# Kernel tuning notes

Hardware: AMD Instinct MI355X
Metric: run time of the kernel (lower is better)

## Reference

```python
import jax, jax.numpy as jnp
import numpy as np

B, C, H, W = 32, 512, 32, 32
HEADS = 8
HD = C // HEADS  # 64
BN_EPS = 1e-5


def setup_inputs() -> dict:
    key = jax.random.key(0)
    ks = jax.random.split(key, 8)
    s = 0.02  # trunc_normal std for Linear weights
    x = jax.random.normal(ks[0], (B, C, H, W), jnp.float32)
    Wq = jax.random.normal(ks[1], (C, C), jnp.float32) * s
    Wk = jax.random.normal(ks[2], (C, C), jnp.float32) * s
    Wv = jax.random.normal(ks[3], (C, C), jnp.float32) * s
    # depthwise 3x3 kernel, kaiming fan_out (fan_out = 3*3*1 per group)
    dw_w = jax.random.normal(ks[4], (C, 1, 3, 3), jnp.float32) * np.sqrt(2.0 / 9.0)
    bn_gamma = jnp.ones((C,), jnp.float32)
    bn_beta = jnp.zeros((C,), jnp.float32)
    temperature = jnp.ones((HEADS, 1, 1), jnp.float32)
    Wp = jax.random.normal(ks[5], (C, C), jnp.float32) * s
    bp = jnp.zeros((C,), jnp.float32)
    return {"x": x, "Wq": Wq, "Wk": Wk, "Wv": Wv, "dw_w": dw_w,
            "bn_gamma": bn_gamma, "bn_beta": bn_beta,
            "temperature": temperature, "Wp": Wp, "bp": bp}


def _l2norm(t):
    # torch F.normalize: x / max(||x||, eps)
    n = jnp.sqrt(jnp.sum(t * t, axis=-1, keepdims=True))
    return t / jnp.maximum(n, 1e-12)


def _forward(x, Wq, Wk, Wv, dw_w, bn_gamma, bn_beta, temperature, Wp, bp):
    b, c, h, w = x.shape
    n = h * w
    x_flat = x.transpose(0, 2, 3, 1).reshape(b, n, c)  # [B,N,C]

    q = (x_flat @ Wq.T).reshape(b, n, HEADS, HD).transpose(0, 2, 3, 1)  # [B,h,d,N]
    k = (x_flat @ Wk.T).reshape(b, n, HEADS, HD).transpose(0, 2, 3, 1)
    q = _l2norm(q)
    k = _l2norm(k)

    attn = jnp.einsum('bhdn,bhen->bhde', q, k) * temperature  # [B,h,d,d]
    attn = jax.nn.softmax(attn, axis=-1)

    v_content = x_flat @ Wv.T  # [B,N,C]

    # gated value path: DWConv -> BatchNorm (batch stats, train mode) -> SiLU
    g = jax.lax.conv_general_dilated(
        x, dw_w, window_strides=(1, 1), padding=((1, 1), (1, 1)),
        feature_group_count=c, dimension_numbers=('NCHW', 'OIHW', 'NCHW'))
    mu = jnp.mean(g, axis=(0, 2, 3), keepdims=True)
    var = jnp.var(g, axis=(0, 2, 3), keepdims=True)
    g = (g - mu) * jax.lax.rsqrt(var + BN_EPS)
    g = g * bn_gamma[None, :, None, None] + bn_beta[None, :, None, None]
    g = g * jax.nn.sigmoid(g)  # SiLU
    v_gate = g.transpose(0, 2, 3, 1).reshape(b, n, c)

    v = (v_content * v_gate).reshape(b, n, HEADS, HD).transpose(0, 2, 3, 1)  # [B,h,d,N]
    out = jnp.einsum('bhde,bhen->bhdn', attn, v)  # [B,h,d,N]
    out = out.transpose(0, 3, 1, 2).reshape(b, n, c)  # [B,N,C]
    out = out @ Wp.T + bp
    return out.reshape(b, h, w, c).transpose(0, 3, 1, 2)  # [B,C,H,W]


def reference(x, Wq, Wk, Wv, dw_w, bn_gamma, bn_beta, temperature, Wp, bp):
    return _forward(x, Wq, Wk, Wv, dw_w, bn_gamma, bn_beta, temperature, Wp, bp)
```

## Files before the change

kernel.cpp:

```cpp
#include <hip/hip_runtime.h>
#include <stdint.h>

#define BATCH 32
#define CCH   512
#define NPIX  1024
#define HEADS 8
#define QKV_M 1536

typedef short bf16x8 __attribute__((ext_vector_type(8)));
typedef float f32x4 __attribute__((ext_vector_type(4)));

__device__ inline float bf2f(unsigned short u) {
  union { float f; uint32_t i; } t; t.i = ((uint32_t)u) << 16; return t.f;
}
__device__ inline unsigned short f2bf(float f) {
  union { float f; uint32_t u; } t; t.f = f;
  uint32_t u = t.u;
  return (unsigned short)((u + 0x7FFFu + ((u >> 16) & 1u)) >> 16);
}

__device__ inline void gl_lds16(const unsigned short* g, unsigned short* l) {
  __builtin_amdgcn_global_load_lds(
      (const __attribute__((address_space(1))) uint32_t*)g,
      (__attribute__((address_space(3))) uint32_t*)l, 16, 0, 0);
}

__global__ void convert_w(const float* __restrict__ Wq, const float* __restrict__ Wk,
                          const float* __restrict__ Wv, const float* __restrict__ Wp,
                          unsigned short* __restrict__ wcat,
                          unsigned short* __restrict__ wpb) {
  int i = (blockIdx.x * 256 + threadIdx.x) * 4;
  union { ushort4 u4; unsigned short s[4]; } o;
  f32x4 a;
  a = *(const f32x4*)&Wq[i];
  for (int j = 0; j < 4; j++) o.s[j] = f2bf(a[j]);
  *(ushort4*)&wcat[i] = o.u4;
  a = *(const f32x4*)&Wk[i];
  for (int j = 0; j < 4; j++) o.s[j] = f2bf(a[j]);
  *(ushort4*)&wcat[CCH * CCH + i] = o.u4;
  a = *(const f32x4*)&Wv[i];
  for (int j = 0; j < 4; j++) o.s[j] = f2bf(a[j]);
  *(ushort4*)&wcat[2 * CCH * CCH + i] = o.u4;
  a = *(const f32x4*)&Wp[i];
  for (int j = 0; j < 4; j++) o.s[j] = f2bf(a[j]);
  *(ushort4*)&wpb[i] = o.u4;
}

__global__ void transpose_f2b(const float* __restrict__ in,
                              unsigned short* __restrict__ out, int R, int Cc) {
  __shared__ float tile[32][33];
  int b = blockIdx.z;
  int c0 = blockIdx.x * 32;
  int r0 = blockIdx.y * 32;
  const float* inb = in + (size_t)b * R * Cc;
  unsigned short* outb = out + (size_t)b * R * Cc;
  int tx = threadIdx.x, ty = threadIdx.y;
  for (int i = 0; i < 4; i++) {
    int r = ty + i * 8;
    tile[r][tx] = inb[(size_t)(r0 + r) * Cc + c0 + tx];
  }
  __syncthreads();
  for (int i = 0; i < 4; i++) {
    int r = ty + i * 8;
    outb[(size_t)(c0 + r) * R + r0 + tx] = f2bf(tile[tx][r]);
  }
}

template <bool OUT_F32>
__launch_bounds__(256)
__global__ void gemm_bt(const unsigned short* __restrict__ A,
                        const unsigned short* __restrict__ X,
                        void* __restrict__ Cout,
                        const float* __restrict__ bias,
                        int M, int N, int K) {
  __shared__ __align__(16) unsigned short As[128 * 64];
  __shared__ __align__(16) unsigned short Bs[128 * 64];
  int b  = blockIdx.z;
  int m0 = blockIdx.y * 128;
  int n0 = blockIdx.x * 128;
  const unsigned short* Xb = X + (size_t)b * N * K;
  int tid = threadIdx.x;
  int lane = tid & 63;
  int wave = tid >> 6;
  int wm = wave >> 1, wn = wave & 1;
  int quad = lane >> 4, l16 = lane & 15;

  f32x4 acc[4][4];
  f32x4 zero = {0.f, 0.f, 0.f, 0.f};
  for (int i = 0; i < 4; i++)
    for (int j = 0; j < 4; j++) acc[i][j] = zero;

  int r8 = lane >> 3;
  int sw = ((lane & 7) ^ r8) * 8;
  const unsigned short* Ag = A  + (size_t)(m0 + wave * 32 + r8) * K + sw;
  const unsigned short* Xg = Xb + (size_t)(n0 + wave * 32 + r8) * K + sw;
  unsigned short* Al = &As[wave * 32 * 64];
  unsigned short* Bl = &Bs[wave * 32 * 64];

  for (int k0 = 0; k0 < K; k0 += 64) {
    for (int i = 0; i < 4; i++) {
      gl_lds16(Ag + k0 + i * 8 * K, Al + i * 8 * 64);
      gl_lds16(Xg + k0 + i * 8 * K, Bl + i * 8 * 64);
    }
    __syncthreads();
    bf16x8 af[2][4], bfr[2][4];
    for (int ks = 0; ks < 2; ks++)
      for (int i = 0; i < 4; i++) {
        int ch = ((ks * 4 + quad) ^ (l16 & 7)) * 8;
        af[ks][i]  = *(const bf16x8*)&As[(wm * 64 + i * 16 + l16) * 64 + ch];
        bfr[ks][i] = *(const bf16x8*)&Bs[(wn * 64 + i * 16 + l16) * 64 + ch];
      }
    for (int ks = 0; ks < 2; ks++)
      for (int i = 0; i < 4; i++)
        for (int j = 0; j < 4; j++)
          acc[i][j] = __builtin_amdgcn_mfma_f32_16x16x32_bf16(
              af[ks][i], bfr[ks][j], acc[i][j], 0, 0, 0);
    __syncthreads();
  }

  for (int i = 0; i < 4; i++) {
    int gmb = m0 + wm * 64 + i * 16 + quad * 4;
    for (int j = 0; j < 4; j++) {
      int gn = n0 + wn * 64 + j * 16 + l16;
      for (int r = 0; r < 4; r++) {
        int gm = gmb + r;
        float v = acc[i][j][r];
        if (OUT_F32) {
          v += bias[gm];
          ((float*)Cout)[(size_t)b * M * N + (size_t)gm * N + gn] = v;
        } else {
          ((unsigned short*)Cout)[(size_t)b * M * N + (size_t)gm * N + gn] = f2bf(v);
        }
      }
    }
  }
}

__global__ void dw_stats(const float* __restrict__ x,
                         const float* __restrict__ wgt,
                         float* __restrict__ s1, float* __restrict__ s2) {
  int c = blockIdx.x, b = blockIdx.y;
  __shared__ __align__(16) float plane[NPIX];
  const float* xp = x + ((size_t)b * CCH + c) * NPIX;
  *(f32x4*)&plane[threadIdx.x * 4] = *(const f32x4*)&xp[threadIdx.x * 4];
  __syncthreads();
  float w[9];
  for (int i = 0; i < 9; i++) w[i] = wgt[c * 9 + i];
  float a1 = 0.f, a2 = 0.f;
  for (int pi = 0; pi < 4; pi++) {
    int p = threadIdx.x + pi * 256;
    int h = p >> 5, wc = p & 31;
    float v = 0.f;
    for (int dh = -1; dh <= 1; dh++)
      for (int dw = -1; dw <= 1; dw++) {
        int hh = h + dh, ww = wc + dw;
        if (hh >= 0 && hh < 32 && ww >= 0 && ww < 32)
          v += w[(dh + 1) * 3 + dw + 1] * plane[hh * 32 + ww];
      }
    a1 += v; a2 += v * v;
  }
  for (int off = 32; off > 0; off >>= 1) {
    a1 += __shfl_down(a1, off);
    a2 += __shfl_down(a2, off);
  }
  __shared__ float r1[4], r2[4];
  int wv = threadIdx.x >> 6;
  if ((threadIdx.x & 63) == 0) { r1[wv] = a1; r2[wv] = a2; }
  __syncthreads();
  if (threadIdx.x == 0) {
    atomicAdd(&s1[c], r1[0] + r1[1] + r1[2] + r1[3]);
    atomicAdd(&s2[c], r2[0] + r2[1] + r2[2] + r2[3]);
  }
}

__global__ void gate_apply(const float* __restrict__ x,
                           const float* __restrict__ wgt,
                           const float* __restrict__ s1, const float* __restrict__ s2,
                           const float* __restrict__ gamma,
                           const float* __restrict__ beta,
                           unsigned short* __restrict__ qkv) {
  int c = blockIdx.x, b = blockIdx.y;
  __shared__ __align__(16) float plane[NPIX];
  const float* xp = x + ((size_t)b * CCH + c) * NPIX;
  unsigned short* vp = qkv + ((size_t)b * QKV_M + 2 * CCH + c) * NPIX;
  *(f32x4*)&plane[threadIdx.x * 4] = *(const f32x4*)&xp[threadIdx.x * 4];
  __syncthreads();
  float w[9];
  for (int i = 0; i < 9; i++) w[i] = wgt[c * 9 + i];
  const float invn = 1.f / 32768.f;
  float mean = s1[c] * invn;
  float var = fmaxf(s2[c] * invn - mean * mean, 0.f);
  float rstd = rsqrtf(var + 1e-5f);
  float ga = gamma[c], be = beta[c];
  for (int pi = 0; pi < 4; pi++) {
    int p = threadIdx.x + pi * 256;
    int h = p >> 5, wc = p & 31;
    float val = 0.f;
    for (int dh = -1; dh <= 1; dh++)
      for (int dw = -1; dw <= 1; dw++) {
        int hh = h + dh, ww = wc + dw;
        if (hh >= 0 && hh < 32 && ww >= 0 && ww < 32)
          val += w[(dh + 1) * 3 + dw + 1] * plane[hh * 32 + ww];
      }
    float g = (val - mean) * rstd * ga + be;
    float sg = g / (1.f + __expf(-g));
    vp[p] = f2bf(bf2f(vp[p]) * sg);
  }
}

__launch_bounds__(256)
__global__ void attn_s(const unsigned short* __restrict__ qkv,
                       const float* __restrict__ temp,
                       unsigned short* __restrict__ P) {
  int bh = blockIdx.x;
  int b = bh >> 3, h = bh & 7;
  const unsigned short* Q = qkv + ((size_t)b * QKV_M + h * 64) * NPIX;
  const unsigned short* K = Q + (size_t)CCH * NPIX;
  int tid = threadIdx.x, lane = tid & 63, wave = tid >> 6;
  int quad = lane >> 4, l16 = lane & 15;

  __shared__ __align__(16) float Sf[64][65];
  __shared__ float qq[64], kk[64], invq[64], invk[64];
  __shared__ float redm[4][64], reds[4][64];

  f32x4 zero = {0.f, 0.f, 0.f, 0.f};
  f32x4 acc[4], accQ = zero, accK = zero;
  for (int j = 0; j < 4; j++) acc[j] = zero;
  for (int n0 = 0; n0 < NPIX; n0 += 32) {
    bf16x8 a  = *(const bf16x8*)&Q[(size_t)(wave * 16 + l16) * NPIX + n0 + quad * 8];
    bf16x8 ak = *(const bf16x8*)&K[(size_t)(wave * 16 + l16) * NPIX + n0 + quad * 8];
    accQ = __builtin_amdgcn_mfma_f32_16x16x32_bf16(a, a, accQ, 0, 0, 0);
    accK = __builtin_amdgcn_mfma_f32_16x16x32_bf16(ak, ak, accK, 0, 0, 0);
    for (int j = 0; j < 4; j++) {
      bf16x8 bb = *(const bf16x8*)&K[(size_t)(j * 16 + l16) * NPIX + n0 + quad * 8];
      acc[j] = __builtin_amdgcn_mfma_f32_16x16x32_bf16(a, bb, acc[j], 0, 0, 0);
    }
  }
  for (int j = 0; j < 4; j++)
    for (int r = 0; r < 4; r++)
      Sf[wave * 16 + quad * 4 + r][j * 16 + l16] = acc[j][r];
  for (int r = 0; r < 4; r++)
    if (l16 == quad * 4 + r) {
      qq[wave * 16 + l16] = accQ[r];
      kk[wave * 16 + l16] = accK[r];
    }
  __syncthreads();
  if (tid < 64) invq[tid] = 1.f / fmaxf(sqrtf(qq[tid]), 1e-12f);
  else if (tid < 128) invk[tid - 64] = 1.f / fmaxf(sqrtf(kk[tid - 64]), 1e-12f);
  __syncthreads();

  int row = tid & 63, seg = tid >> 6;
  float fq = temp[h] * invq[row];
  float v[16], pm = -1e30f;
  for (int i = 0; i < 16; i++) {
    v[i] = Sf[row][seg * 16 + i] * fq * invk[seg * 16 + i];
    pm = fmaxf(pm, v[i]);
  }
  redm[seg][row] = pm;
  __syncthreads();
  float m = fmaxf(fmaxf(redm[0][row], redm[1][row]),
                  fmaxf(redm[2][row], redm[3][row]));
  float ps = 0.f;
  for (int i = 0; i < 16; i++) { v[i] = __expf(v[i] - m); ps += v[i]; }
  reds[seg][row] = ps;
  __syncthreads();
  float inv = 1.f / (reds[0][row] + reds[1][row] + reds[2][row] + reds[3][row]);
  union { uint4 q4[2]; unsigned short s[16]; } u;
  for (int i = 0; i < 16; i++) u.s[i] = f2bf(v[i] * inv);
  unsigned short* Pp = P + ((size_t)bh * 64 + row) * 64 + seg * 16;
  *(uint4*)&Pp[0] = u.q4[0];
  *(uint4*)&Pp[8] = u.q4[1];
}

__launch_bounds__(256)
__global__ void attn_o(const unsigned short* __restrict__ qkv,
                       const unsigned short* __restrict__ P,
                       unsigned short* __restrict__ aoT) {
  int blk = blockIdx.x;
  int nc = blk & 3, bh = blk >> 2;
  int b = bh >> 3, h = bh & 7;
  const unsigned short* V = qkv + ((size_t)b * QKV_M + 2 * CCH + h * 64) * NPIX;
  unsigned short* Ob = aoT + (size_t)b * NPIX * CCH + h * 64;
  int tid = threadIdx.x, lane = tid & 63, wave = tid >> 6;
  int quad = lane >> 4, l16 = lane & 15;

  __shared__ __align__(16) unsigned short Vt[4][16][72];
  __shared__ __align__(16) unsigned short Ot[4][16][72];

  const unsigned short* Pb = P + (size_t)bh * 64 * 64;
  bf16x8 Pf[4][2];
  for (int j = 0; j < 4; j++)
    for (int ks = 0; ks < 2; ks++)
      Pf[j][ks] = *(const bf16x8*)&Pb[(j * 16 + l16) * 64 + ks * 32 + quad * 8];

  f32x4 zero = {0.f, 0.f, 0.f, 0.f};
  int e1 = lane >> 1, noff = (lane & 1) * 8;
  int nbase = nc * 256 + wave * 64;
  int orow = lane >> 3, ocol = (lane & 7) * 8;

  union { uint4 q; unsigned short s[8]; } g0, g1, c0, c1;
  g0.q = *(const uint4*)&V[(size_t)e1 * NPIX + nbase + noff];
  g1.q = *(const uint4*)&V[(size_t)(e1 + 32) * NPIX + nbase + noff];
#pragma unroll
  for (int nt = 0; nt < 4; nt++) {
    int n0 = nbase + nt * 16;
    c0 = g0; c1 = g1;
    if (nt < 3) {
      g0.q = *(const uint4*)&V[(size_t)e1 * NPIX + n0 + 16 + noff];
      g1.q = *(const uint4*)&V[(size_t)(e1 + 32) * NPIX + n0 + 16 + noff];
    }
    for (int jj = 0; jj < 8; jj++) {
      Vt[wave][noff + jj][e1]      = c0.s[jj];
      Vt[wave][noff + jj][e1 + 32] = c1.s[jj];
    }
    bf16x8 Af0 = *(const bf16x8*)&Vt[wave][l16][quad * 8];
    bf16x8 Af1 = *(const bf16x8*)&Vt[wave][l16][32 + quad * 8];
    f32x4 oacc[4];
    for (int j = 0; j < 4; j++) {
      oacc[j] = __builtin_amdgcn_mfma_f32_16x16x32_bf16(Af0, Pf[j][0], zero, 0, 0, 0);
      oacc[j] = __builtin_amdgcn_mfma_f32_16x16x32_bf16(Af1, Pf[j][1], oacc[j], 0, 0, 0);
    }
    for (int j = 0; j < 4; j++)
      for (int r = 0; r < 4; r++)
        Ot[wave][quad * 4 + r][j * 16 + l16] = f2bf(oacc[j][r]);
    uint4 o0 = *(const uint4*)&Ot[wave][orow][ocol];
    uint4 o1 = *(const uint4*)&Ot[wave][orow + 8][ocol];
    *(uint4*)&Ob[(size_t)(n0 + orow) * CCH + ocol] = o0;
    *(uint4*)&Ob[(size_t)(n0 + orow + 8) * CCH + ocol] = o1;
  }
}

extern "C" void kernel_launch(void* const* d_in, const int* in_sizes, int n_in,
                              void* d_out, int out_size, void* d_ws, size_t ws_size,
                              hipStream_t stream) {
  const float* x     = (const float*)d_in[0];
  const float* Wq    = (const float*)d_in[1];
  const float* Wk    = (const float*)d_in[2];
  const float* Wv    = (const float*)d_in[3];
  const float* dww   = (const float*)d_in[4];
  const float* gamma = (const float*)d_in[5];
  const float* beta  = (const float*)d_in[6];
  const float* temp  = (const float*)d_in[7];
  const float* Wp    = (const float*)d_in[8];
  const float* bp    = (const float*)d_in[9];
  float* out = (float*)d_out;

  char* ws = (char*)d_ws;
  unsigned short* wcat = (unsigned short*)ws;
  unsigned short* wpb  = wcat + (size_t)QKV_M * CCH;
  float* s1 = (float*)(wpb + (size_t)CCH * CCH);
  float* s2 = s1 + CCH;
  unsigned short* Pbuf = (unsigned short*)(s2 + CCH);
  char* dyn = (char*)(Pbuf + (size_t)BATCH * HEADS * 64 * 64);
  size_t fixed = (size_t)(dyn - ws);
  size_t per_b = ((size_t)NPIX * CCH + (size_t)QKV_M * NPIX) * 2;
  int BC = BATCH;
  while (BC > 1 && fixed + (size_t)BC * per_b > ws_size) BC >>= 1;
  unsigned short* xT  = (unsigned short*)dyn;
  unsigned short* qkv = xT + (size_t)BC * NPIX * CCH;

  convert_w<<<CCH * CCH / 1024, 256, 0, stream>>>(Wq, Wk, Wv, Wp, wcat, wpb);
  hipMemsetAsync(s1, 0, 2 * CCH * sizeof(float), stream);
  dw_stats<<<dim3(CCH, BATCH), 256, 0, stream>>>(x, dww, s1, s2);

  for (int b0 = 0; b0 < BATCH; b0 += BC) {
    const float* xc = x + (size_t)b0 * CCH * NPIX;
    float* outc = out + (size_t)b0 * CCH * NPIX;
    transpose_f2b<<<dim3(NPIX / 32, CCH / 32, BC), dim3(32, 8), 0, stream>>>(
        xc, xT, CCH, NPIX);
    gemm_bt<false><<<dim3(NPIX / 128, QKV_M / 128, BC), 256, 0, stream>>>(
        wcat, xT, qkv, nullptr, QKV_M, NPIX, CCH);
    attn_s<<<BC * HEADS, 256, 0, stream>>>(qkv, temp, Pbuf);
    gate_apply<<<dim3(CCH, BC), 256, 0, stream>>>(xc, dww, s1, s2, gamma, beta, qkv);
    attn_o<<<BC * HEADS * 4, 256, 0, stream>>>(qkv, Pbuf, xT);
    gemm_bt<true><<<dim3(NPIX / 128, CCH / 128, BC), 256, 0, stream>>>(
        wpb, xT, outc, bp, CCH, NPIX, CCH);
  }
}
```

Before: 336.2 us.

## Fuse BN-SiLU gating into QKV GEMM epilogue and split attn_s along N

The depthwise conv output is now stored once as bf16 while the BN statistics are gathered, and a small kernel precomputes the per-channel BN scale and shift. The QKV GEMM uses 256-row tiles and applies the SiLU gate to the V rows in its epilogue, which removes the separate gate_apply pass that recomputed the conv and reread and rewrote V. attn_s now splits the pixel dimension across its four waves and sums the partial scores in shared memory, so each wave has more MFMA work. The cost is an extra bf16 gate buffer of B*C*N elements, more workspace (which can shrink the batch chunk), and higher register pressure in the larger GEMM tile.

```diff
diff --git a/kernel.cpp b/kernel.cpp
--- a/kernel.cpp
+++ b/kernel.cpp
@@ -66,82 +66,14 @@
   }
 }
 
-template <bool OUT_F32>
-__launch_bounds__(256)
-__global__ void gemm_bt(const unsigned short* __restrict__ A,
-                        const unsigned short* __restrict__ X,
-                        void* __restrict__ Cout,
-                        const float* __restrict__ bias,
-                        int M, int N, int K) {
-  __shared__ __align__(16) unsigned short As[128 * 64];
-  __shared__ __align__(16) unsigned short Bs[128 * 64];
-  int b  = blockIdx.z;
-  int m0 = blockIdx.y * 128;
-  int n0 = blockIdx.x * 128;
-  const unsigned short* Xb = X + (size_t)b * N * K;
-  int tid = threadIdx.x;
-  int lane = tid & 63;
-  int wave = tid >> 6;
-  int wm = wave >> 1, wn = wave & 1;
-  int quad = lane >> 4, l16 = lane & 15;
-
-  f32x4 acc[4][4];
-  f32x4 zero = {0.f, 0.f, 0.f, 0.f};
-  for (int i = 0; i < 4; i++)
-    for (int j = 0; j < 4; j++) acc[i][j] = zero;
-
-  int r8 = lane >> 3;
-  int sw = ((lane & 7) ^ r8) * 8;
-  const unsigned short* Ag = A  + (size_t)(m0 + wave * 32 + r8) * K + sw;
-  const unsigned short* Xg = Xb + (size_t)(n0 + wave * 32 + r8) * K + sw;
-  unsigned short* Al = &As[wave * 32 * 64];
-  unsigned short* Bl = &Bs[wave * 32 * 64];
-
-  for (int k0 = 0; k0 < K; k0 += 64) {
-    for (int i = 0; i < 4; i++) {
-      gl_lds16(Ag + k0 + i * 8 * K, Al + i * 8 * 64);
-      gl_lds16(Xg + k0 + i * 8 * K, Bl + i * 8 * 64);
-    }
-    __syncthreads();
-    bf16x8 af[2][4], bfr[2][4];
-    for (int ks = 0; ks < 2; ks++)
-      for (int i = 0; i < 4; i++) {
-        int ch = ((ks * 4 + quad) ^ (l16 & 7)) * 8;
-        af[ks][i]  = *(const bf16x8*)&As[(wm * 64 + i * 16 + l16) * 64 + ch];
-        bfr[ks][i] = *(const bf16x8*)&Bs[(wn * 64 + i * 16 + l16) * 64 + ch];
-      }
-    for (int ks = 0; ks < 2; ks++)
-      for (int i = 0; i < 4; i++)
-        for (int j = 0; j < 4; j++)
-          acc[i][j] = __builtin_amdgcn_mfma_f32_16x16x32_bf16(
-              af[ks][i], bfr[ks][j], acc[i][j], 0, 0, 0);
-    __syncthreads();
-  }
-
-  for (int i = 0; i < 4; i++) {
-    int gmb = m0 + wm * 64 + i * 16 + quad * 4;
-    for (int j = 0; j < 4; j++) {
-      int gn = n0 + wn * 64 + j * 16 + l16;
-      for (int r = 0; r < 4; r++) {
-        int gm = gmb + r;
-        float v = acc[i][j][r];
-        if (OUT_F32) {
-          v += bias[gm];
-          ((float*)Cout)[(size_t)b * M * N + (size_t)gm * N + gn] = v;
-        } else {
-          ((unsigned short*)Cout)[(size_t)b * M * N + (size_t)gm * N + gn] = f2bf(v);
-        }
-      }
-    }
-  }
-}
-
-__global__ void dw_stats(const float* __restrict__ x,
-                         const float* __restrict__ wgt,
-                         float* __restrict__ s1, float* __restrict__ s2) {
+__global__ void conv_store(const float* __restrict__ x,
+                           const float* __restrict__ wgt,
+                           unsigned short* __restrict__ gbuf,
+                           float* __restrict__ s1, float* __restrict__ s2) {
   int c = blockIdx.x, b = blockIdx.y;
   __shared__ __align__(16) float plane[NPIX];
   const float* xp = x + ((size_t)b * CCH + c) * NPIX;
+  unsigned short* gp = gbuf + ((size_t)b * CCH + c) * NPIX;
   *(f32x4*)&plane[threadIdx.x * 4] = *(const f32x4*)&xp[threadIdx.x * 4];
   __syncthreads();
   float w[9];
@@ -158,6 +90,7 @@
           v += w[(dh + 1) * 3 + dw + 1] * plane[hh * 32 + ww];
       }
     a1 += v; a2 += v * v;
+    gp[p] = f2bf(v);
   }
   for (int off = 32; off > 0; off >>= 1) {
     a1 += __shfl_down(a1, off);
@@ -173,38 +106,146 @@
   }
 }
 
-__global__ void gate_apply(const float* __restrict__ x,
-                           const float* __restrict__ wgt,
-                           const float* __restrict__ s1, const float* __restrict__ s2,
-                           const float* __restrict__ gamma,
-                           const float* __restrict__ beta,
-                           unsigned short* __restrict__ qkv) {
-  int c = blockIdx.x, b = blockIdx.y;
-  __shared__ __align__(16) float plane[NPIX];
-  const float* xp = x + ((size_t)b * CCH + c) * NPIX;
-  unsigned short* vp = qkv + ((size_t)b * QKV_M + 2 * CCH + c) * NPIX;
-  *(f32x4*)&plane[threadIdx.x * 4] = *(const f32x4*)&xp[threadIdx.x * 4];
-  __syncthreads();
-  float w[9];
-  for (int i = 0; i < 9; i++) w[i] = wgt[c * 9 + i];
+__global__ void bn_coef(const float* __restrict__ s1, const float* __restrict__ s2,
+                        const float* __restrict__ gamma, const float* __restrict__ beta,
+                        float2* __restrict__ coef) {
+  int c = blockIdx.x * 256 + threadIdx.x;
   const float invn = 1.f / 32768.f;
   float mean = s1[c] * invn;
   float var = fmaxf(s2[c] * invn - mean * mean, 0.f);
-  float rstd = rsqrtf(var + 1e-5f);
-  float ga = gamma[c], be = beta[c];
-  for (int pi = 0; pi < 4; pi++) {
-    int p = threadIdx.x + pi * 256;
-    int h = p >> 5, wc = p & 31;
-    float val = 0.f;
-    for (int dh = -1; dh <= 1; dh++)
-      for (int dw = -1; dw <= 1; dw++) {
-        int hh = h + dh, ww = wc + dw;
-        if (hh >= 0 && hh < 32 && ww >= 0 && ww < 32)
-          val += w[(dh + 1) * 3 + dw + 1] * plane[hh * 32 + ww];
+  float sc = gamma[c] * rsqrtf(var + 1e-5f);
+  coef[c] = make_float2(sc, beta[c] - mean * sc);
+}
+
+__launch_bounds__(256, 2)
+__global__ void gemm_qkv(const unsigned short* __restrict__ A,
+                         const unsigned short* __restrict__ X,
+                         unsigned short* __restrict__ Cout,
+                         const unsigned short* __restrict__ gbuf,
+                         const float2* __restrict__ coef,
+                         int N, int K) {
+  __shared__ __align__(16) unsigned short As[256 * 64];
+  __shared__ __align__(16) unsigned short Bs[128 * 64];
+  int b  = blockIdx.z;
+  int m0 = blockIdx.y * 256;
+  int n0 = blockIdx.x * 128;
+  const unsigned short* Xb = X + (size_t)b * N * K;
+  int tid = threadIdx.x;
+  int lane = tid & 63;
+  int wave = tid >> 6;
+  int wm = wave >> 1, wn = wave & 1;
+  int quad = lane >> 4, l16 = lane & 15;
+
+  f32x4 acc[8][4];
+  f32x4 zero = {0.f, 0.f, 0.f, 0.f};
+  for (int i = 0; i < 8; i++)
+    for (int j = 0; j < 4; j++) acc[i][j] = zero;
+
+  int r8 = lane >> 3;
+  int sw = ((lane & 7) ^ r8) * 8;
+  const unsigned short* Ag = A  + (size_t)(m0 + wave * 64 + r8) * K + sw;
+  const unsigned short* Xg = Xb + (size_t)(n0 + wave * 32 + r8) * K + sw;
+  unsigned short* Al = &As[wave * 64 * 64];
+  unsigned short* Bl = &Bs[wave * 32 * 64];
+
+  for (int k0 = 0; k0 < K; k0 += 64) {
+    for (int i = 0; i < 8; i++) gl_lds16(Ag + k0 + i * 8 * K, Al + i * 8 * 64);
+    for (int i = 0; i < 4; i++) gl_lds16(Xg + k0 + i * 8 * K, Bl + i * 8 * 64);
+    __syncthreads();
+    for (int ks = 0; ks < 2; ks++) {
+      int ch = ((ks * 4 + quad) ^ (l16 & 7)) * 8;
+      bf16x8 af[8], bfr[4];
+      for (int i = 0; i < 8; i++)
+        af[i] = *(const bf16x8*)&As[(wm * 128 + i * 16 + l16) * 64 + ch];
+      for (int j = 0; j < 4; j++)
+        bfr[j] = *(const bf16x8*)&Bs[(wn * 64 + j * 16 + l16) * 64 + ch];
+      for (int i = 0; i < 8; i++)
+        for (int j = 0; j < 4; j++)
+          acc[i][j] = __builtin_amdgcn_mfma_f32_16x16x32_bf16(af[i], bfr[j], acc[i][j], 0, 0, 0);
+    }
+    __syncthreads();
+  }
+
+  bool gate = (m0 >= 2 * CCH);
+  for (int i = 0; i < 8; i++) {
+    int gm0 = m0 + wm * 128 + i * 16 + quad * 4;
+    for (int r = 0; r < 4; r++) {
+      int gm = gm0 + r;
+      float sc = 0.f, sh = 0.f;
+      if (gate) { float2 cf = coef[gm - 2 * CCH]; sc = cf.x; sh = cf.y; }
+      for (int j = 0; j < 4; j++) {
+        int gn = n0 + wn * 64 + j * 16 + l16;
+        float v = acc[i][j][r];
+        if (gate) {
+          float gg = bf2f(gbuf[((size_t)b * CCH + (gm - 2 * CCH)) * NPIX + gn]);
+          float gi = gg * sc + sh;
+          v *= gi / (1.f + __expf(-gi));
+        }
+        Cout[(size_t)b * QKV_M * N + (size_t)gm * N + gn] = f2bf(v);
       }
-    float g = (val - mean) * rstd * ga + be;
-    float sg = g / (1.f + __expf(-g));
-    vp[p] = f2bf(bf2f(vp[p]) * sg);
+    }
+  }
+}
+
+__launch_bounds__(256)
+__global__ void gemm_proj(const unsigned short* __restrict__ A,
+                          const unsigned short* __restrict__ X,
+                          float* __restrict__ Cout,
+                          const float* __restrict__ bias,
+                          int M, int N, int K) {
+  __shared__ __align__(16) unsigned short As[128 * 64];
+  __shared__ __align__(16) unsigned short Bs[128 * 64];
+  int b  = blockIdx.z;
+  int m0 = blockIdx.y * 128;
+  int n0 = blockIdx.x * 128;
+  const unsigned short* Xb = X + (size_t)b * N * K;
+  int tid = threadIdx.x;
+  int lane = tid & 63;
+  int wave = tid >> 6;
+  int wm = wave >> 1, wn = wave & 1;
+  int quad = lane >> 4, l16 = lane & 15;
+
+  f32x4 acc[4][4];
+  f32x4 zero = {0.f, 0.f, 0.f, 0.f};
+  for (int i = 0; i < 4; i++)
+    for (int j = 0; j < 4; j++) acc[i][j] = zero;
+
+  int r8 = lane >> 3;
+  int sw = ((lane & 7) ^ r8) * 8;
+  const unsigned short* Ag = A  + (size_t)(m0 + wave * 32 + r8) * K + sw;
+  const unsigned short* Xg = Xb + (size_t)(n0 + wave * 32 + r8) * K + sw;
+  unsigned short* Al = &As[wave * 32 * 64];
+  unsigned short* Bl = &Bs[wave * 32 * 64];
+
+  for (int k0 = 0; k0 < K; k0 += 64) {
+    for (int i = 0; i < 4; i++) {
+      gl_lds16(Ag + k0 + i * 8 * K, Al + i * 8 * 64);
+      gl_lds16(Xg + k0 + i * 8 * K, Bl + i * 8 * 64);
+    }
+    __syncthreads();
+    for (int ks = 0; ks < 2; ks++) {
+      int ch = ((ks * 4 + quad) ^ (l16 & 7)) * 8;
+      bf16x8 af[4], bfr[4];
+      for (int i = 0; i < 4; i++) {
+        af[i]  = *(const bf16x8*)&As[(wm * 64 + i * 16 + l16) * 64 + ch];
+        bfr[i] = *(const bf16x8*)&Bs[(wn * 64 + i * 16 + l16) * 64 + ch];
+      }
+      for (int i = 0; i < 4; i++)
+        for (int j = 0; j < 4; j++)
+          acc[i][j] = __builtin_amdgcn_mfma_f32_16x16x32_bf16(af[i], bfr[j], acc[i][j], 0, 0, 0);
+    }
+    __syncthreads();
+  }
+
+  for (int i = 0; i < 4; i++) {
+    int gmb = m0 + wm * 64 + i * 16 + quad * 4;
+    for (int j = 0; j < 4; j++) {
+      int gn = n0 + wn * 64 + j * 16 + l16;
+      for (int r = 0; r < 4; r++) {
+        int gm = gmb + r;
+        Cout[(size_t)b * M * N + (size_t)gm * N + gn] = acc[i][j][r] + bias[gm];
+      }
+    }
   }
 }
 
@@ -219,41 +260,58 @@
   int tid = threadIdx.x, lane = tid & 63, wave = tid >> 6;
   int quad = lane >> 4, l16 = lane & 15;
 
-  __shared__ __align__(16) float Sf[64][65];
-  __shared__ float qq[64], kk[64], invq[64], invk[64];
+  __shared__ float Sp[4][64][68];
+  __shared__ float qqp[4][64], kkp[4][64];
   __shared__ float redm[4][64], reds[4][64];
+  __shared__ float invq[64], invk[64];
 
   f32x4 zero = {0.f, 0.f, 0.f, 0.f};
-  f32x4 acc[4], accQ = zero, accK = zero;
-  for (int j = 0; j < 4; j++) acc[j] = zero;
-  for (int n0 = 0; n0 < NPIX; n0 += 32) {
-    bf16x8 a  = *(const bf16x8*)&Q[(size_t)(wave * 16 + l16) * NPIX + n0 + quad * 8];
-    bf16x8 ak = *(const bf16x8*)&K[(size_t)(wave * 16 + l16) * NPIX + n0 + quad * 8];
-    accQ = __builtin_amdgcn_mfma_f32_16x16x32_bf16(a, a, accQ, 0, 0, 0);
-    accK = __builtin_amdgcn_mfma_f32_16x16x32_bf16(ak, ak, accK, 0, 0, 0);
-    for (int j = 0; j < 4; j++) {
-      bf16x8 bb = *(const bf16x8*)&K[(size_t)(j * 16 + l16) * NPIX + n0 + quad * 8];
-      acc[j] = __builtin_amdgcn_mfma_f32_16x16x32_bf16(a, bb, acc[j], 0, 0, 0);
-    }
-  }
-  for (int j = 0; j < 4; j++)
+  f32x4 acc[4][4], accQ[4], accK[4];
+  for (int i = 0; i < 4; i++) {
+    accQ[i] = zero; accK[i] = zero;
+    for (int j = 0; j < 4; j++) acc[i][j] = zero;
+  }
+  for (int nc = 0; nc < 8; nc++) {
+    int n0 = wave * 256 + nc * 32;
+    bf16x8 qa[4], ka[4];
+    for (int i = 0; i < 4; i++) {
+      qa[i] = *(const bf16x8*)&Q[(size_t)(i * 16 + l16) * NPIX + n0 + quad * 8];
+      ka[i] = *(const bf16x8*)&K[(size_t)(i * 16 + l16) * NPIX + n0 + quad * 8];
+    }
+    for (int i = 0; i < 4; i++) {
+      accQ[i] = __builtin_amdgcn_mfma_f32_16x16x32_bf16(qa[i], qa[i], accQ[i], 0, 0, 0);
+      accK[i] = __builtin_amdgcn_mfma_f32_16x16x32_bf16(ka[i], ka[i], accK[i], 0, 0, 0);
+    }
+    for (int i = 0; i < 4; i++)
+      for (int j = 0; j < 4; j++)
+        acc[i][j] = __builtin_amdgcn_mfma_f32_16x16x32_bf16(qa[i], ka[j], acc[i][j], 0, 0, 0);
+  }
+  for (int i = 0; i < 4; i++)
+    for (int j = 0; j < 4; j++)
+      for (int r = 0; r < 4; r++)
+        Sp[wave][i * 16 + quad * 4 + r][j * 16 + l16] = acc[i][j][r];
+  for (int i = 0; i < 4; i++)
     for (int r = 0; r < 4; r++)
-      Sf[wave * 16 + quad * 4 + r][j * 16 + l16] = acc[j][r];
-  for (int r = 0; r < 4; r++)
-    if (l16 == quad * 4 + r) {
-      qq[wave * 16 + l16] = accQ[r];
-      kk[wave * 16 + l16] = accK[r];
-    }
-  __syncthreads();
-  if (tid < 64) invq[tid] = 1.f / fmaxf(sqrtf(qq[tid]), 1e-12f);
-  else if (tid < 128) invk[tid - 64] = 1.f / fmaxf(sqrtf(kk[tid - 64]), 1e-12f);
+      if (l16 == quad * 4 + r) {
+        qqp[wave][i * 16 + l16] = accQ[i][r];
+        kkp[wave][i * 16 + l16] = accK[i][r];
+      }
+  __syncthreads();
+  if (tid < 64)
+    invq[tid] = 1.f / fmaxf(sqrtf(qqp[0][tid] + qqp[1][tid] + qqp[2][tid] + qqp[3][tid]), 1e-12f);
+  else if (tid < 128) {
+    int t = tid - 64;
+    invk[t] = 1.f / fmaxf(sqrtf(kkp[0][t] + kkp[1][t] + kkp[2][t] + kkp[3][t]), 1e-12f);
+  }
   __syncthreads();
 
   int row = tid & 63, seg = tid >> 6;
   float fq = temp[h] * invq[row];
   float v[16], pm = -1e30f;
   for (int i = 0; i < 16; i++) {
-    v[i] = Sf[row][seg * 16 + i] * fq * invk[seg * 16 + i];
+    int e = seg * 16 + i;
+    float sv = Sp[0][row][e] + Sp[1][row][e] + Sp[2][row][e] + Sp[3][row][e];
+    v[i] = sv * fq * invk[e];
     pm = fmaxf(pm, v[i]);
   }
   redm[seg][row] = pm;
@@ -350,8 +408,10 @@
   unsigned short* wpb  = wcat + (size_t)QKV_M * CCH;
   float* s1 = (float*)(wpb + (size_t)CCH * CCH);
   float* s2 = s1 + CCH;
-  unsigned short* Pbuf = (unsigned short*)(s2 + CCH);
-  char* dyn = (char*)(Pbuf + (size_t)BATCH * HEADS * 64 * 64);
+  float2* coef = (float2*)(s2 + CCH);
+  unsigned short* Pbuf = (unsigned short*)(coef + CCH);
+  unsigned short* gbuf = Pbuf + (size_t)BATCH * HEADS * 64 * 64;
+  char* dyn = (char*)(gbuf + (size_t)BATCH * CCH * NPIX);
   size_t fixed = (size_t)(dyn - ws);
   size_t per_b = ((size_t)NPIX * CCH + (size_t)QKV_M * NPIX) * 2;
   int BC = BATCH;
@@ -361,19 +421,20 @@
 
   convert_w<<<CCH * CCH / 1024, 256, 0, stream>>>(Wq, Wk, Wv, Wp, wcat, wpb);
   hipMemsetAsync(s1, 0, 2 * CCH * sizeof(float), stream);
-  dw_stats<<<dim3(CCH, BATCH), 256, 0, stream>>>(x, dww, s1, s2);
+  conv_store<<<dim3(CCH, BATCH), 256, 0, stream>>>(x, dww, gbuf, s1, s2);
+  bn_coef<<<CCH / 256, 256, 0, stream>>>(s1, s2, gamma, beta, coef);
 
   for (int b0 = 0; b0 < BATCH; b0 += BC) {
     const float* xc = x + (size_t)b0 * CCH * NPIX;
     float* outc = out + (size_t)b0 * CCH * NPIX;
+    const unsigned short* gc = gbuf + (size_t)b0 * CCH * NPIX;
     transpose_f2b<<<dim3(NPIX / 32, CCH / 32, BC), dim3(32, 8), 0, stream>>>(
         xc, xT, CCH, NPIX);
-    gemm_bt<false><<<dim3(NPIX / 128, QKV_M / 128, BC), 256, 0, stream>>>(
-        wcat, xT, qkv, nullptr, QKV_M, NPIX, CCH);
+    gemm_qkv<<<dim3(NPIX / 128, QKV_M / 256, BC), 256, 0, stream>>>(
+        wcat, xT, qkv, gc, coef, NPIX, CCH);
     attn_s<<<BC * HEADS, 256, 0, stream>>>(qkv, temp, Pbuf);
-    gate_apply<<<dim3(CCH, BC), 256, 0, stream>>>(xc, dww, s1, s2, gamma, beta, qkv);
     attn_o<<<BC * HEADS * 4, 256, 0, stream>>>(qkv, Pbuf, xT);
-    gemm_bt<true><<<dim3(NPIX / 128, CCH / 128, BC), 256, 0, stream>>>(
+    gemm_proj<<<dim3(NPIX / 128, CCH / 128, BC), 256, 0, stream>>>(
         wpb, xT, outc, bp, CCH, NPIX, CCH);
   }
 }
```

New measurement: 338.5 us. About the same (+0.7%).
